# Performance work log

Hardware: AMD Instinct MI355X
Metric: run time of the kernel (lower is better)

Reference implementation:

```python
import jax, jax.numpy as jnp
import numpy as np

N = 50000      # num_nodes
E = 800000     # num_edges
D = 128        # hidden_dim
V = 32000      # vocab_size
T = 8          # num_edge_types
NT = 16        # num_node_types


def setup_inputs() -> dict:
    key = jax.random.key(0)
    ks = jax.random.split(key, 10)
    s = 1.0 / np.sqrt(D)
    return {
        "x": jax.random.randint(ks[0], (N,), 0, V),
        "edge_index": jax.random.randint(ks[1], (2, E), 0, N),
        "edge_type": jax.random.randint(ks[2], (E,), 0, T),
        "node_type": jax.random.randint(ks[3], (N,), 0, NT),
        "emb": jax.random.normal(ks[4], (V, D), dtype=jnp.float32) * s,
        "W_rel": jax.random.normal(ks[5], (T, D, D), dtype=jnp.float32) * s,
        "b_node": jax.random.normal(ks[6], (NT, D), dtype=jnp.float32) * 0.01,
        "W_ih": jax.random.normal(ks[7], (3 * D, D), dtype=jnp.float32) * s,
        "W_hh": jax.random.normal(ks[8], (3 * D, D), dtype=jnp.float32) * s,
        "b_ih": jnp.zeros((3 * D,), dtype=jnp.float32),
        "b_hh": jnp.zeros((3 * D,), dtype=jnp.float32),
    }


def _gru_cell(inp, h, W_ih, W_hh, b_ih, b_hh):
    # torch.nn.GRUCell semantics
    gi = inp @ W_ih.T + b_ih   # [N, 3D]
    gh = h @ W_hh.T + b_hh     # [N, 3D]
    i_r, i_z, i_n = jnp.split(gi, 3, axis=-1)
    h_r, h_z, h_n = jnp.split(gh, 3, axis=-1)
    r = jax.nn.sigmoid(i_r + h_r)
    z = jax.nn.sigmoid(i_z + h_z)
    n = jnp.tanh(i_n + r * h_n)
    return (1.0 - z) * n + z * h


def reference(x, edge_index, edge_type, node_type, emb, W_rel, b_node, W_ih, W_hh, b_ih, b_hh):
    h = emb[x]                                   # [N, D] node embeddings
    src, dst = edge_index[0], edge_index[1]
    n_nodes = h.shape[0]
    for _ in range(5):
        # relational message passing: per-edge-type linear on source nodes
        Ht = jnp.einsum('nd,tdf->ntf', h, W_rel)  # [N, T, D] all-type transforms
        msg = Ht[src, edge_type]                  # [E, D] gather per edge
        aggr = jax.ops.segment_sum(msg, dst, num_segments=n_nodes)  # scatter-add to dst
        aggr = aggr + b_node[node_type]           # node-type-specific bias
        h = _gru_cell(aggr, h, W_ih, W_hh, b_ih, b_hh)
    return h
```

## Files before the change

### kernel.cpp

```cpp
#include <hip/hip_runtime.h>
#include <hip/hip_fp16.h>
#include <math.h>

#define N_NODES 50000
#define N_EDGES 800000
#define D 128
#define T_TYPES 8
#define TPAD 136
#define NBLK_SCAN 196
#define TILES 1563
#define GRID_GRU 512

typedef short short8 __attribute__((ext_vector_type(8)));
typedef unsigned short ushort4v __attribute__((ext_vector_type(4)));
typedef float float4v __attribute__((ext_vector_type(4)));
typedef unsigned short ushort_t;

static __device__ __forceinline__ unsigned short f2bf(float f) {
    unsigned u = __float_as_uint(f);
    u += 0x7fff + ((u >> 16) & 1);
    return (unsigned short)(u >> 16);
}
static __device__ __forceinline__ float bf2f(unsigned short b) {
    return __uint_as_float((unsigned)b << 16);
}
static __device__ __forceinline__ void splitbf(float x, unsigned short& hi, unsigned short& lo) {
    unsigned short h_ = f2bf(x);
    hi = h_;
    lo = f2bf(x - bf2f(h_));
}

#define GLOAD16(gp, lp) __builtin_amdgcn_global_load_lds( \
    (const __attribute__((address_space(1))) unsigned int*)(gp), \
    (__attribute__((address_space(3))) unsigned int*)(lp), 16, 0, 0)

__global__ void embed_gather(const int* __restrict__ x, const float* __restrict__ emb,
                             ushort_t* __restrict__ hhi, ushort_t* __restrict__ hlo) {
    int n = blockIdx.x;
    int d = threadIdx.x;
    float v = emb[(size_t)x[n] * D + d];
    unsigned short a, b;
    splitbf(v, a, b);
    hhi[(size_t)n * D + d] = a;
    hlo[(size_t)n * D + d] = b;
}

__global__ void convert_wrelT(const float* __restrict__ Wrel,
                              ushort_t* __restrict__ hi, ushort_t* __restrict__ lo) {
    int idx = blockIdx.x * 256 + threadIdx.x;
    int t = idx >> 14;
    int rem = idx & 16383;
    int f = rem >> 7;
    int d = rem & 127;
    unsigned short a, b;
    splitbf(Wrel[((size_t)t << 14) + (d << 7) + f], a, b);
    hi[idx] = a;
    lo[idx] = b;
}

__global__ void convert_w(const float* __restrict__ in,
                          ushort_t* __restrict__ hi, ushort_t* __restrict__ lo, int n) {
    int idx = blockIdx.x * 256 + threadIdx.x;
    if (idx < n) {
        unsigned short a, b;
        splitbf(in[idx], a, b);
        hi[idx] = a;
        lo[idx] = b;
    }
}

__global__ void count_deg(const int* __restrict__ ei, int* __restrict__ deg) {
    int e = blockIdx.x * 256 + threadIdx.x;
    if (e >= N_EDGES) return;
    atomicAdd(&deg[ei[N_EDGES + e]], 1);
}

__global__ __launch_bounds__(256) void scan_blocks(const int* __restrict__ deg,
                                                   int* __restrict__ bsums) {
    __shared__ int red[4];
    int idx = blockIdx.x * 256 + threadIdx.x;
    int v = (idx < N_NODES) ? deg[idx] : 0;
#pragma unroll
    for (int o = 32; o > 0; o >>= 1) v += __shfl_down(v, o);
    if ((threadIdx.x & 63) == 0) red[threadIdx.x >> 6] = v;
    __syncthreads();
    if (threadIdx.x == 0) bsums[blockIdx.x] = red[0] + red[1] + red[2] + red[3];
}

__global__ __launch_bounds__(256) void scan_tops(int* __restrict__ bsums) {
    __shared__ int s[256];
    int tid = threadIdx.x;
    int v = (tid < NBLK_SCAN) ? bsums[tid] : 0;
    s[tid] = v;
    __syncthreads();
#pragma unroll
    for (int o = 1; o < 256; o <<= 1) {
        int u = (tid >= o) ? s[tid - o] : 0;
        __syncthreads();
        s[tid] += u;
        __syncthreads();
    }
    if (tid < NBLK_SCAN) bsums[tid] = s[tid] - v;
}

__global__ __launch_bounds__(256) void scan_final(const int* __restrict__ bsums,
                                                  int* __restrict__ deg_cursor,
                                                  int* __restrict__ rs) {
    __shared__ int s[256];
    int tid = threadIdx.x;
    int idx = blockIdx.x * 256 + tid;
    int v = (idx < N_NODES) ? deg_cursor[idx] : 0;
    s[tid] = v;
    __syncthreads();
#pragma unroll
    for (int o = 1; o < 256; o <<= 1) {
        int u = (tid >= o) ? s[tid - o] : 0;
        __syncthreads();
        s[tid] += u;
        __syncthreads();
    }
    int excl = s[tid] - v + bsums[blockIdx.x];
    if (idx < N_NODES) {
        rs[idx] = excl;
        deg_cursor[idx] = excl;
    }
    if (idx == 0) rs[N_NODES] = N_EDGES;
}

__global__ void fill_csr(const int* __restrict__ ei, const int* __restrict__ et,
                         int* __restrict__ cursor, int* __restrict__ packed) {
    int e = blockIdx.x * 256 + threadIdx.x;
    if (e >= N_EDGES) return;
    int dst = ei[N_EDGES + e];
    int pos = atomicAdd(&cursor[dst], 1);
    packed[pos] = (ei[e] << 3) | et[e];
}

__global__ __launch_bounds__(256, 2) void gemm_rel(const ushort_t* __restrict__ hhi,
                                                   const ushort_t* __restrict__ hlo,
                                                   const ushort_t* __restrict__ Whi,
                                                   const ushort_t* __restrict__ Wlo,
                                                   ushort_t* __restrict__ Ht) {
    __shared__ __align__(16) ushort_t wlds[2][128 * TPAD];
    const int tid = threadIdx.x;
    const int wave = tid >> 6, lane = tid & 63;
    const int q = lane >> 4, li = lane & 15;
    const int t = blockIdx.y;
    const int m_base = blockIdx.x * 128 + wave * 32;

    {
        const ushort_t* gh = Whi + ((size_t)t << 14);
        const ushort_t* gl = Wlo + ((size_t)t << 14);
#pragma unroll
        for (int i = 0; i < 8; ++i) {
            int g = (i * 256 + tid) * 8;
            int row = g >> 7, col = g & 127;
            *(short8*)(&wlds[0][row * TPAD + col]) = *(const short8*)(gh + g);
            *(short8*)(&wlds[1][row * TPAD + col]) = *(const short8*)(gl + g);
        }
    }
    __syncthreads();

    int r0 = m_base + li;      if (r0 > N_NODES - 1) r0 = N_NODES - 1;
    int r1 = m_base + 16 + li; if (r1 > N_NODES - 1) r1 = N_NODES - 1;
    const ushort_t* A0h = hhi + (size_t)r0 * D + q * 8;
    const ushort_t* A0l = hlo + (size_t)r0 * D + q * 8;
    const ushort_t* A1h = hhi + (size_t)r1 * D + q * 8;
    const ushort_t* A1l = hlo + (size_t)r1 * D + q * 8;

    short8 a0h[4], a0l[4], a1h[4], a1l[4];
#pragma unroll
    for (int ks = 0; ks < 4; ++ks) {
        a0h[ks] = *(const short8*)(A0h + ks * 32);
        a0l[ks] = *(const short8*)(A0l + ks * 32);
        a1h[ks] = *(const short8*)(A1h + ks * 32);
        a1l[ks] = *(const short8*)(A1l + ks * 32);
    }

    float4v acc[2][8];
#pragma unroll
    for (int m = 0; m < 2; ++m)
#pragma unroll
        for (int ft = 0; ft < 8; ++ft) acc[m][ft] = (float4v){0.f, 0.f, 0.f, 0.f};

#pragma unroll
    for (int ks = 0; ks < 4; ++ks) {
#pragma unroll
        for (int ft = 0; ft < 8; ++ft) {
            const int lo_off = (ft * 16 + li) * TPAD + ks * 32 + q * 8;
            short8 bh = *(const short8*)(&wlds[0][lo_off]);
            short8 bl = *(const short8*)(&wlds[1][lo_off]);
            acc[0][ft] = __builtin_amdgcn_mfma_f32_16x16x32_bf16(a0h[ks], bh, acc[0][ft], 0, 0, 0);
            acc[0][ft] = __builtin_amdgcn_mfma_f32_16x16x32_bf16(a0l[ks], bh, acc[0][ft], 0, 0, 0);
            acc[0][ft] = __builtin_amdgcn_mfma_f32_16x16x32_bf16(a0h[ks], bl, acc[0][ft], 0, 0, 0);
            acc[1][ft] = __builtin_amdgcn_mfma_f32_16x16x32_bf16(a1h[ks], bh, acc[1][ft], 0, 0, 0);
            acc[1][ft] = __builtin_amdgcn_mfma_f32_16x16x32_bf16(a1l[ks], bh, acc[1][ft], 0, 0, 0);
            acc[1][ft] = __builtin_amdgcn_mfma_f32_16x16x32_bf16(a1h[ks], bl, acc[1][ft], 0, 0, 0);
        }
    }

    __syncthreads();
    ushort_t* tw = &wlds[0][0] + wave * 32 * TPAD;
#pragma unroll
    for (int m = 0; m < 2; ++m)
#pragma unroll
        for (int ft = 0; ft < 8; ++ft)
#pragma unroll
            for (int r = 0; r < 4; ++r) {
                __half hv = __float2half_rn(acc[m][ft][r]);
                tw[(m * 16 + q * 4 + r) * TPAD + ft * 16 + li] = __half_as_ushort(hv);
            }
#pragma unroll
    for (int i = 0; i < 8; ++i) {
        int row = i * 4 + q;
        int col = li * 8;
        short8 v = *(const short8*)(tw + row * TPAD + col);
        int orow = m_base + row;
        if (orow < N_NODES)
            *(short8*)(Ht + (size_t)orow * 1024 + (t << 7) + col) = v;
    }
}

__global__ __launch_bounds__(256) void aggregate_csr(const int* __restrict__ rs,
                                                     const int* __restrict__ packed,
                                                     const ushort_t* __restrict__ Ht,
                                                     const int* __restrict__ nt,
                                                     const float* __restrict__ b_node,
                                                     ushort_t* __restrict__ ahi,
                                                     ushort_t* __restrict__ alo) {
    int n = blockIdx.x * 4 + (threadIdx.x >> 6);
    if (n >= N_NODES) return;
    const int lane = threadIdx.x & 63;
    const int beg = rs[n], end = rs[n + 1];
    const __half2* Ht2 = (const __half2*)Ht;

    float2 acc = ((const float2*)(b_node + (size_t)nt[n] * D))[lane];

    int i = beg;
    for (; i + 3 < end; i += 4) {
        int p0 = packed[i], p1 = packed[i + 1], p2 = packed[i + 2], p3 = packed[i + 3];
        float2 f0 = __half22float2(Ht2[(size_t)p0 * 64 + lane]);
        float2 f1 = __half22float2(Ht2[(size_t)p1 * 64 + lane]);
        float2 f2 = __half22float2(Ht2[(size_t)p2 * 64 + lane]);
        float2 f3 = __half22float2(Ht2[(size_t)p3 * 64 + lane]);
        acc.x += (f0.x + f1.x) + (f2.x + f3.x);
        acc.y += (f0.y + f1.y) + (f2.y + f3.y);
    }
    for (; i < end; ++i) {
        int pk = packed[i];
        float2 fv = __half22float2(Ht2[(size_t)pk * 64 + lane]);
        acc.x += fv.x;
        acc.y += fv.y;
    }

    unsigned short h0, l0, h1, l1;
    splitbf(acc.x, h0, l0);
    splitbf(acc.y, h1, l1);
    ((unsigned*)ahi)[(size_t)n * 64 + lane] = (unsigned)h0 | ((unsigned)h1 << 16);
    ((unsigned*)alo)[(size_t)n * 64 + lane] = (unsigned)l0 | ((unsigned)l1 << 16);
}

__global__ __launch_bounds__(512, 2) void gru_persist(
    const ushort_t* __restrict__ ahi, const ushort_t* __restrict__ alo,
    const ushort_t* __restrict__ hhi_in, const ushort_t* __restrict__ hlo_in,
    ushort_t* __restrict__ hhi_out, ushort_t* __restrict__ hlo_out,
    const ushort_t* __restrict__ Wihi, const ushort_t* __restrict__ Wilo,
    const ushort_t* __restrict__ Whhi, const ushort_t* __restrict__ Whlo,
    const float* __restrict__ b_ih, const float* __restrict__ b_hh,
    float* __restrict__ h, int write_h)
{
    __shared__ __align__(16) ushort_t xlds[2][4][4096];

    const int tid = threadIdx.x;
    const int w = tid >> 6, lane = tid & 63;
    const int q = lane >> 4, li = lane & 15;
    const int fg = w * 16 + li;
    const int f0 = w * 16 + q * 4;

    const size_t oR = (size_t)fg * D + q * 8;
    const size_t oZ = (size_t)(D + fg) * D + q * 8;
    const size_t oN = (size_t)(2 * D + fg) * D + q * 8;
    short8 Wr[12][4];
#pragma unroll
    for (int ks = 0; ks < 4; ++ks) {
        const int off = ks * 32;
        Wr[0][ks]  = *(const short8*)(Wihi + oR + off);
        Wr[1][ks]  = *(const short8*)(Wilo + oR + off);
        Wr[2][ks]  = *(const short8*)(Whhi + oR + off);
        Wr[3][ks]  = *(const short8*)(Whlo + oR + off);
        Wr[4][ks]  = *(const short8*)(Wihi + oZ + off);
        Wr[5][ks]  = *(const short8*)(Wilo + oZ + off);
        Wr[6][ks]  = *(const short8*)(Whhi + oZ + off);
        Wr[7][ks]  = *(const short8*)(Whlo + oZ + off);
        Wr[8][ks]  = *(const short8*)(Wihi + oN + off);
        Wr[9][ks]  = *(const short8*)(Wilo + oN + off);
        Wr[10][ks] = *(const short8*)(Whhi + oN + off);
        Wr[11][ks] = *(const short8*)(Whlo + oN + off);
    }
    float4v bR4 = *(const float4v*)(b_ih + f0);
    float4v bZ4 = *(const float4v*)(b_ih + D + f0);
    float4v bIn4 = *(const float4v*)(b_ih + 2 * D + f0);
    {
        float4v t0 = *(const float4v*)(b_hh + f0);
        float4v t1 = *(const float4v*)(b_hh + D + f0);
        bR4 += t0; bZ4 += t1;
    }
    float4v bHn4 = *(const float4v*)(b_hh + 2 * D + f0);

    const int lrow = w * 4 + (lane >> 4);
    const int cswz = (lane & 15) ^ (lrow & 7);

#define STAGE(BUF_, TILE_) do {                                      \
        int gr_ = (TILE_) * 32 + lrow;                               \
        if (gr_ > N_NODES - 1) gr_ = N_NODES - 1;                    \
        const size_t so_ = (size_t)gr_ * D + cswz * 8;               \
        ushort_t* lb_ = &xlds[BUF_][0][0] + (w * 4) * 128;           \
        GLOAD16(ahi + so_,    lb_);                                  \
        GLOAD16(alo + so_,    lb_ + 4096);                           \
        GLOAD16(hhi_in + so_, lb_ + 8192);                           \
        GLOAD16(hlo_in + so_, lb_ + 12288);                          \
    } while (0)

    const int s = blockIdx.x;
    STAGE(0, s);
    __syncthreads();

    int cur = 0;
    for (int tile = s; tile < TILES; tile += GRID_GRU) {
        const int nxt = tile + GRID_GRU;
        if (nxt < TILES) STAGE(cur ^ 1, nxt);

        const ushort_t* xb = &xlds[cur][0][0];
        float4v aR[2], aZ[2], aI[2], aH[2];
#pragma unroll
        for (int m = 0; m < 2; ++m) {
            aR[m] = (float4v){0.f, 0.f, 0.f, 0.f};
            aZ[m] = aR[m]; aI[m] = aR[m]; aH[m] = aR[m];
        }
#pragma unroll
        for (int ks = 0; ks < 4; ++ks) {
#pragma unroll
            for (int m = 0; m < 2; ++m) {
                const int row = m * 16 + li;
                const int inoff = row * 128 + ((ks * 32 + q * 8) ^ ((row & 7) << 3));
                short8 xah = *(const short8*)(xb + inoff);
                short8 xal = *(const short8*)(xb + 4096 + inoff);
                short8 xhh = *(const short8*)(xb + 8192 + inoff);
                short8 xhl = *(const short8*)(xb + 12288 + inoff);
                aR[m] = __builtin_amdgcn_mfma_f32_16x16x32_bf16(Wr[0][ks], xah, aR[m], 0, 0, 0);
                aR[m] = __builtin_amdgcn_mfma_f32_16x16x32_bf16(Wr[0][ks], xal, aR[m], 0, 0, 0);
                aR[m] = __builtin_amdgcn_mfma_f32_16x16x32_bf16(Wr[1][ks], xah, aR[m], 0, 0, 0);
                aR[m] = __builtin_amdgcn_mfma_f32_16x16x32_bf16(Wr[2][ks], xhh, aR[m], 0, 0, 0);
                aR[m] = __builtin_amdgcn_mfma_f32_16x16x32_bf16(Wr[2][ks], xhl, aR[m], 0, 0, 0);
                aR[m] = __builtin_amdgcn_mfma_f32_16x16x32_bf16(Wr[3][ks], xhh, aR[m], 0, 0, 0);
                aZ[m] = __builtin_amdgcn_mfma_f32_16x16x32_bf16(Wr[4][ks], xah, aZ[m], 0, 0, 0);
                aZ[m] = __builtin_amdgcn_mfma_f32_16x16x32_bf16(Wr[4][ks], xal, aZ[m], 0, 0, 0);
                aZ[m] = __builtin_amdgcn_mfma_f32_16x16x32_bf16(Wr[5][ks], xah, aZ[m], 0, 0, 0);
                aZ[m] = __builtin_amdgcn_mfma_f32_16x16x32_bf16(Wr[6][ks], xhh, aZ[m], 0, 0, 0);
                aZ[m] = __builtin_amdgcn_mfma_f32_16x16x32_bf16(Wr[6][ks], xhl, aZ[m], 0, 0, 0);
                aZ[m] = __builtin_amdgcn_mfma_f32_16x16x32_bf16(Wr[7][ks], xhh, aZ[m], 0, 0, 0);
                aI[m] = __builtin_amdgcn_mfma_f32_16x16x32_bf16(Wr[8][ks], xah, aI[m], 0, 0, 0);
                aI[m] = __builtin_amdgcn_mfma_f32_16x16x32_bf16(Wr[8][ks], xal, aI[m], 0, 0, 0);
                aI[m] = __builtin_amdgcn_mfma_f32_16x16x32_bf16(Wr[9][ks], xah, aI[m], 0, 0, 0);
                aH[m] = __builtin_amdgcn_mfma_f32_16x16x32_bf16(Wr[10][ks], xhh, aH[m], 0, 0, 0);
                aH[m] = __builtin_amdgcn_mfma_f32_16x16x32_bf16(Wr[10][ks], xhl, aH[m], 0, 0, 0);
                aH[m] = __builtin_amdgcn_mfma_f32_16x16x32_bf16(Wr[11][ks], xhh, aH[m], 0, 0, 0);
            }
        }

#pragma unroll
        for (int m = 0; m < 2; ++m) {
            const int node = tile * 32 + m * 16 + li;
            const int row = m * 16 + li;
            const int chunk = (f0 >> 3) ^ (row & 7);
            const int hoff = row * 128 + chunk * 8 + (q & 1) * 4;
            ushort4v hh4 = *(const ushort4v*)(xb + 8192 + hoff);
            ushort4v hl4 = *(const ushort4v*)(xb + 12288 + hoff);
            if (node < N_NODES) {
                ushort4v sh4, sl4;
                float4v hn4;
#pragma unroll
                for (int r = 0; r < 4; ++r) {
                    float hold = bf2f(hh4[r]) + bf2f(hl4[r]);
                    float rg = 1.0f / (1.0f + __expf(-(aR[m][r] + bR4[r])));
                    float zg = 1.0f / (1.0f + __expf(-(aZ[m][r] + bZ4[r])));
                    float narg = aI[m][r] + bIn4[r] + rg * (aH[m][r] + bHn4[r]);
                    float ex = __expf(2.0f * narg);
                    float ng = 1.0f - 2.0f / (ex + 1.0f);
                    float hn = (1.0f - zg) * ng + zg * hold;
                    hn4[r] = hn;
                    unsigned short sh, sl;
                    splitbf(hn, sh, sl);
                    sh4[r] = sh;
                    sl4[r] = sl;
                }
                const size_t go = (size_t)node * D + f0;
                *(ushort4v*)(hhi_out + go) = sh4;
                *(ushort4v*)(hlo_out + go) = sl4;
                if (write_h) *(float4v*)(h + go) = hn4;
            }
        }
        __syncthreads();
        cur ^= 1;
    }
#undef STAGE
}

extern "C" void kernel_launch(void* const* d_in, const int* in_sizes, int n_in,
                              void* d_out, int out_size, void* d_ws, size_t ws_size,
                              hipStream_t stream) {
    const int* x      = (const int*)d_in[0];
    const int* ei     = (const int*)d_in[1];
    const int* et     = (const int*)d_in[2];
    const int* nt     = (const int*)d_in[3];
    const float* emb  = (const float*)d_in[4];
    const float* Wrel = (const float*)d_in[5];
    const float* b_node = (const float*)d_in[6];
    const float* W_ih = (const float*)d_in[7];
    const float* W_hh = (const float*)d_in[8];
    const float* b_ih = (const float*)d_in[9];
    const float* b_hh = (const float*)d_in[10];

    float* h = (float*)d_out;
    float* ws = (float*)d_ws;

    ushort_t* Ht = (ushort_t*)ws;
    ushort_t* us = (ushort_t*)(ws + 25600000);
    ushort_t* ahi  = us;
    ushort_t* alo  = us + 6400000;
    ushort_t* hhi  = us + 12800000;
    ushort_t* hlo  = us + 19200000;
    ushort_t* Whi  = us + 25600000;
    ushort_t* Wlo  = Whi + 131072;
    ushort_t* Wihi = Wlo + 131072;
    ushort_t* Wilo = Wihi + 49152;
    ushort_t* Whhi = Wilo + 49152;
    ushort_t* Whlo = Whhi + 49152;
    int* rs     = (int*)(ws + 38629376);
    int* packed = rs + 50004;
    int* bsums  = packed + 800000;
    ushort_t* hhi2 = (ushort_t*)(ws + 39479808);
    ushort_t* hlo2 = hhi2 + 6400000;
    int* deg    = (int*)ws;

    convert_wrelT<<<512, 256, 0, stream>>>(Wrel, Whi, Wlo);
    convert_w<<<192, 256, 0, stream>>>(W_ih, Wihi, Wilo, 3 * D * D);
    convert_w<<<192, 256, 0, stream>>>(W_hh, Whhi, Whlo, 3 * D * D);
    embed_gather<<<N_NODES, 128, 0, stream>>>(x, emb, hhi, hlo);

    hipMemsetAsync(deg, 0, 50000 * sizeof(int), stream);
    count_deg<<<3125, 256, 0, stream>>>(ei, deg);
    scan_blocks<<<NBLK_SCAN, 256, 0, stream>>>(deg, bsums);
    scan_tops<<<1, 256, 0, stream>>>(bsums);
    scan_final<<<NBLK_SCAN, 256, 0, stream>>>(bsums, deg, rs);
    fill_csr<<<3125, 256, 0, stream>>>(ei, et, deg, packed);

    for (int it = 0; it < 5; ++it) {
        const ushort_t* hi_in = (it & 1) ? hhi2 : hhi;
        const ushort_t* lo_in = (it & 1) ? hlo2 : hlo;
        ushort_t* hi_out = (it & 1) ? hhi : hhi2;
        ushort_t* lo_out = (it & 1) ? hlo : hlo2;
        dim3 g(391, T_TYPES);
        gemm_rel<<<g, 256, 0, stream>>>(hi_in, lo_in, Whi, Wlo, Ht);
        aggregate_csr<<<12500, 256, 0, stream>>>(rs, packed, Ht, nt, b_node, ahi, alo);
        gru_persist<<<GRID_GRU, 512, 0, stream>>>(ahi, alo, hi_in, lo_in, hi_out, lo_out,
                                                  Wihi, Wilo, Whhi, Whlo, b_ih, b_hh,
                                                  h, it == 4 ? 1 : 0);
    }
}
```

Before: 1.055 ms.

## Store Ht in type-major planes, drop LDS staging in relational GEMM and GRU

The per-type transform output Ht moves from node-major [N,T,D] to type-major planes [T,N,D], and the CSR packed edge index becomes et*N+src so the aggregation gather addresses the new layout directly. The relational GEMM no longer stages W_rel into LDS; it reads weight fragments straight from global/cache, which shrinks LDS so the launch bound can allow 4 blocks per CU. The persistent double-buffered GRU kernel with register-resident weights is replaced by a non-persistent 2D grid that reloads weights and inputs from global memory per tile. The aim is higher occupancy and less LDS/sync overhead, at the cost of more global/L2 traffic for weights.

```diff
diff --git a/kernel.cpp b/kernel.cpp
--- a/kernel.cpp
+++ b/kernel.cpp
@@ -9,7 +9,7 @@
 #define TPAD 136
 #define NBLK_SCAN 196
 #define TILES 1563
-#define GRID_GRU 512
+#define HT_PLANE 6400000
 
 typedef short short8 __attribute__((ext_vector_type(8)));
 typedef unsigned short ushort4v __attribute__((ext_vector_type(4)));
@@ -29,10 +29,6 @@
     hi = h_;
     lo = f2bf(x - bf2f(h_));
 }
-
-#define GLOAD16(gp, lp) __builtin_amdgcn_global_load_lds( \
-    (const __attribute__((address_space(1))) unsigned int*)(gp), \
-    (__attribute__((address_space(3))) unsigned int*)(lp), 16, 0, 0)
 
 __global__ void embed_gather(const int* __restrict__ x, const float* __restrict__ emb,
                              ushort_t* __restrict__ hhi, ushort_t* __restrict__ hlo) {
@@ -133,33 +129,20 @@
     if (e >= N_EDGES) return;
     int dst = ei[N_EDGES + e];
     int pos = atomicAdd(&cursor[dst], 1);
-    packed[pos] = (ei[e] << 3) | et[e];
-}
-
-__global__ __launch_bounds__(256, 2) void gemm_rel(const ushort_t* __restrict__ hhi,
+    packed[pos] = et[e] * N_NODES + ei[e];
+}
+
+__global__ __launch_bounds__(256, 4) void gemm_rel(const ushort_t* __restrict__ hhi,
                                                    const ushort_t* __restrict__ hlo,
                                                    const ushort_t* __restrict__ Whi,
                                                    const ushort_t* __restrict__ Wlo,
                                                    ushort_t* __restrict__ Ht) {
-    __shared__ __align__(16) ushort_t wlds[2][128 * TPAD];
+    __shared__ __align__(16) ushort_t twb[4][32 * TPAD];
     const int tid = threadIdx.x;
     const int wave = tid >> 6, lane = tid & 63;
     const int q = lane >> 4, li = lane & 15;
     const int t = blockIdx.y;
     const int m_base = blockIdx.x * 128 + wave * 32;
-
-    {
-        const ushort_t* gh = Whi + ((size_t)t << 14);
-        const ushort_t* gl = Wlo + ((size_t)t << 14);
-#pragma unroll
-        for (int i = 0; i < 8; ++i) {
-            int g = (i * 256 + tid) * 8;
-            int row = g >> 7, col = g & 127;
-            *(short8*)(&wlds[0][row * TPAD + col]) = *(const short8*)(gh + g);
-            *(short8*)(&wlds[1][row * TPAD + col]) = *(const short8*)(gl + g);
-        }
-    }
-    __syncthreads();
 
     int r0 = m_base + li;      if (r0 > N_NODES - 1) r0 = N_NODES - 1;
     int r1 = m_base + 16 + li; if (r1 > N_NODES - 1) r1 = N_NODES - 1;
@@ -183,13 +166,15 @@
 #pragma unroll
         for (int ft = 0; ft < 8; ++ft) acc[m][ft] = (float4v){0.f, 0.f, 0.f, 0.f};
 
+    const ushort_t* Wth = Whi + ((size_t)t << 14);
+    const ushort_t* Wtl = Wlo + ((size_t)t << 14);
 #pragma unroll
     for (int ks = 0; ks < 4; ++ks) {
 #pragma unroll
         for (int ft = 0; ft < 8; ++ft) {
-            const int lo_off = (ft * 16 + li) * TPAD + ks * 32 + q * 8;
-            short8 bh = *(const short8*)(&wlds[0][lo_off]);
-            short8 bl = *(const short8*)(&wlds[1][lo_off]);
+            const int wo = (ft * 16 + li) * 128 + ks * 32 + q * 8;
+            short8 bh = *(const short8*)(Wth + wo);
+            short8 bl = *(const short8*)(Wtl + wo);
             acc[0][ft] = __builtin_amdgcn_mfma_f32_16x16x32_bf16(a0h[ks], bh, acc[0][ft], 0, 0, 0);
             acc[0][ft] = __builtin_amdgcn_mfma_f32_16x16x32_bf16(a0l[ks], bh, acc[0][ft], 0, 0, 0);
             acc[0][ft] = __builtin_amdgcn_mfma_f32_16x16x32_bf16(a0h[ks], bl, acc[0][ft], 0, 0, 0);
@@ -199,8 +184,7 @@
         }
     }
 
-    __syncthreads();
-    ushort_t* tw = &wlds[0][0] + wave * 32 * TPAD;
+    ushort_t* tw = &twb[wave][0];
 #pragma unroll
     for (int m = 0; m < 2; ++m)
 #pragma unroll
@@ -217,7 +201,7 @@
         short8 v = *(const short8*)(tw + row * TPAD + col);
         int orow = m_base + row;
         if (orow < N_NODES)
-            *(short8*)(Ht + (size_t)orow * 1024 + (t << 7) + col) = v;
+            *(short8*)(Ht + (size_t)t * HT_PLANE + (size_t)orow * D + col) = v;
     }
 }
 
@@ -260,7 +244,7 @@
     ((unsigned*)alo)[(size_t)n * 64 + lane] = (unsigned)l0 | ((unsigned)l1 << 16);
 }
 
-__global__ __launch_bounds__(512, 2) void gru_persist(
+__global__ __launch_bounds__(256, 4) void gru_direct(
     const ushort_t* __restrict__ ahi, const ushort_t* __restrict__ alo,
     const ushort_t* __restrict__ hhi_in, const ushort_t* __restrict__ hlo_in,
     ushort_t* __restrict__ hhi_out, ushort_t* __restrict__ hlo_out,
@@ -269,34 +253,17 @@
     const float* __restrict__ b_ih, const float* __restrict__ b_hh,
     float* __restrict__ h, int write_h)
 {
-    __shared__ __align__(16) ushort_t xlds[2][4][4096];
-
     const int tid = threadIdx.x;
     const int w = tid >> 6, lane = tid & 63;
     const int q = lane >> 4, li = lane & 15;
-    const int fg = w * 16 + li;
-    const int f0 = w * 16 + q * 4;
+    const int fg = blockIdx.y * 64 + w * 16 + li;
+    const int f0 = blockIdx.y * 64 + w * 16 + q * 4;
+    const int n0 = blockIdx.x * 32;
 
     const size_t oR = (size_t)fg * D + q * 8;
     const size_t oZ = (size_t)(D + fg) * D + q * 8;
     const size_t oN = (size_t)(2 * D + fg) * D + q * 8;
-    short8 Wr[12][4];
-#pragma unroll
-    for (int ks = 0; ks < 4; ++ks) {
-        const int off = ks * 32;
-        Wr[0][ks]  = *(const short8*)(Wihi + oR + off);
-        Wr[1][ks]  = *(const short8*)(Wilo + oR + off);
-        Wr[2][ks]  = *(const short8*)(Whhi + oR + off);
-        Wr[3][ks]  = *(const short8*)(Whlo + oR + off);
-        Wr[4][ks]  = *(const short8*)(Wihi + oZ + off);
-        Wr[5][ks]  = *(const short8*)(Wilo + oZ + off);
-        Wr[6][ks]  = *(const short8*)(Whhi + oZ + off);
-        Wr[7][ks]  = *(const short8*)(Whlo + oZ + off);
-        Wr[8][ks]  = *(const short8*)(Wihi + oN + off);
-        Wr[9][ks]  = *(const short8*)(Wilo + oN + off);
-        Wr[10][ks] = *(const short8*)(Whhi + oN + off);
-        Wr[11][ks] = *(const short8*)(Whlo + oN + off);
-    }
+
     float4v bR4 = *(const float4v*)(b_ih + f0);
     float4v bZ4 = *(const float4v*)(b_ih + D + f0);
     float4v bIn4 = *(const float4v*)(b_ih + 2 * D + f0);
@@ -307,103 +274,110 @@
     }
     float4v bHn4 = *(const float4v*)(b_hh + 2 * D + f0);
 
-    const int lrow = w * 4 + (lane >> 4);
-    const int cswz = (lane & 15) ^ (lrow & 7);
-
-#define STAGE(BUF_, TILE_) do {                                      \
-        int gr_ = (TILE_) * 32 + lrow;                               \
-        if (gr_ > N_NODES - 1) gr_ = N_NODES - 1;                    \
-        const size_t so_ = (size_t)gr_ * D + cswz * 8;               \
-        ushort_t* lb_ = &xlds[BUF_][0][0] + (w * 4) * 128;           \
-        GLOAD16(ahi + so_,    lb_);                                  \
-        GLOAD16(alo + so_,    lb_ + 4096);                           \
-        GLOAD16(hhi_in + so_, lb_ + 8192);                           \
-        GLOAD16(hlo_in + so_, lb_ + 12288);                          \
-    } while (0)
-
-    const int s = blockIdx.x;
-    STAGE(0, s);
-    __syncthreads();
-
-    int cur = 0;
-    for (int tile = s; tile < TILES; tile += GRID_GRU) {
-        const int nxt = tile + GRID_GRU;
-        if (nxt < TILES) STAGE(cur ^ 1, nxt);
-
-        const ushort_t* xb = &xlds[cur][0][0];
-        float4v aR[2], aZ[2], aI[2], aH[2];
-#pragma unroll
-        for (int m = 0; m < 2; ++m) {
-            aR[m] = (float4v){0.f, 0.f, 0.f, 0.f};
-            aZ[m] = aR[m]; aI[m] = aR[m]; aH[m] = aR[m];
+    int r0 = n0 + li;      if (r0 > N_NODES - 1) r0 = N_NODES - 1;
+    int r1 = n0 + 16 + li; if (r1 > N_NODES - 1) r1 = N_NODES - 1;
+    const size_t xo0 = (size_t)r0 * D + q * 8;
+    const size_t xo1 = (size_t)r1 * D + q * 8;
+
+    float4v aR[2], aZ[2], aI[2], aH[2];
+#pragma unroll
+    for (int m = 0; m < 2; ++m) {
+        aR[m] = (float4v){0.f, 0.f, 0.f, 0.f};
+        aZ[m] = aR[m]; aI[m] = aR[m]; aH[m] = aR[m];
+    }
+
+#pragma unroll
+    for (int ks = 0; ks < 4; ++ks) {
+        const int off = ks * 32;
+        short8 x0ah = *(const short8*)(ahi + xo0 + off);
+        short8 x0al = *(const short8*)(alo + xo0 + off);
+        short8 x0hh = *(const short8*)(hhi_in + xo0 + off);
+        short8 x0hl = *(const short8*)(hlo_in + xo0 + off);
+        short8 x1ah = *(const short8*)(ahi + xo1 + off);
+        short8 x1al = *(const short8*)(alo + xo1 + off);
+        short8 x1hh = *(const short8*)(hhi_in + xo1 + off);
+        short8 x1hl = *(const short8*)(hlo_in + xo1 + off);
+        short8 wIRh = *(const short8*)(Wihi + oR + off);
+        short8 wIRl = *(const short8*)(Wilo + oR + off);
+        short8 wHRh = *(const short8*)(Whhi + oR + off);
+        short8 wHRl = *(const short8*)(Whlo + oR + off);
+        short8 wIZh = *(const short8*)(Wihi + oZ + off);
+        short8 wIZl = *(const short8*)(Wilo + oZ + off);
+        short8 wHZh = *(const short8*)(Whhi + oZ + off);
+        short8 wHZl = *(const short8*)(Whlo + oZ + off);
+        short8 wINh = *(const short8*)(Wihi + oN + off);
+        short8 wINl = *(const short8*)(Wilo + oN + off);
+        short8 wHNh = *(const short8*)(Whhi + oN + off);
+        short8 wHNl = *(const short8*)(Whlo + oN + off);
+
+        aR[0] = __builtin_amdgcn_mfma_f32_16x16x32_bf16(wIRh, x0ah, aR[0], 0, 0, 0);
+        aR[0] = __builtin_amdgcn_mfma_f32_16x16x32_bf16(wIRh, x0al, aR[0], 0, 0, 0);
+        aR[0] = __builtin_amdgcn_mfma_f32_16x16x32_bf16(wIRl, x0ah, aR[0], 0, 0, 0);
+        aR[0] = __builtin_amdgcn_mfma_f32_16x16x32_bf16(wHRh, x0hh, aR[0], 0, 0, 0);
+        aR[0] = __builtin_amdgcn_mfma_f32_16x16x32_bf16(wHRh, x0hl, aR[0], 0, 0, 0);
+        aR[0] = __builtin_amdgcn_mfma_f32_16x16x32_bf16(wHRl, x0hh, aR[0], 0, 0, 0);
+        aZ[0] = __builtin_amdgcn_mfma_f32_16x16x32_bf16(wIZh, x0ah, aZ[0], 0, 0, 0);
+        aZ[0] = __builtin_amdgcn_mfma_f32_16x16x32_bf16(wIZh, x0al, aZ[0], 0, 0, 0);
+        aZ[0] = __builtin_amdgcn_mfma_f32_16x16x32_bf16(wIZl, x0ah, aZ[0], 0, 0, 0);
+        aZ[0] = __builtin_amdgcn_mfma_f32_16x16x32_bf16(wHZh, x0hh, aZ[0], 0, 0, 0);
+        aZ[0] = __builtin_amdgcn_mfma_f32_16x16x32_bf16(wHZh, x0hl, aZ[0], 0, 0, 0);
+        aZ[0] = __builtin_amdgcn_mfma_f32_16x16x32_bf16(wHZl, x0hh, aZ[0], 0, 0, 0);
+        aI[0] = __builtin_amdgcn_mfma_f32_16x16x32_bf16(wINh, x0ah, aI[0], 0, 0, 0);
+        aI[0] = __builtin_amdgcn_mfma_f32_16x16x32_bf16(wINh, x0al, aI[0], 0, 0, 0);
+        aI[0] = __builtin_amdgcn_mfma_f32_16x16x32_bf16(wINl, x0ah, aI[0], 0, 0, 0);
+        aH[0] = __builtin_amdgcn_mfma_f32_16x16x32_bf16(wHNh, x0hh, aH[0], 0, 0, 0);
+        aH[0] = __builtin_amdgcn_mfma_f32_16x16x32_bf16(wHNh, x0hl, aH[0], 0, 0, 0);
+        aH[0] = __builtin_amdgcn_mfma_f32_16x16x32_bf16(wHNl, x0hh, aH[0], 0, 0, 0);
+
+        aR[1] = __builtin_amdgcn_mfma_f32_16x16x32_bf16(wIRh, x1ah, aR[1], 0, 0, 0);
+        aR[1] = __builtin_amdgcn_mfma_f32_16x16x32_bf16(wIRh, x1al, aR[1], 0, 0, 0);
+        aR[1] = __builtin_amdgcn_mfma_f32_16x16x32_bf16(wIRl, x1ah, aR[1], 0, 0, 0);
+        aR[1] = __builtin_amdgcn_mfma_f32_16x16x32_bf16(wHRh, x1hh, aR[1], 0, 0, 0);
+        aR[1] = __builtin_amdgcn_mfma_f32_16x16x32_bf16(wHRh, x1hl, aR[1], 0, 0, 0);
+        aR[1] = __builtin_amdgcn_mfma_f32_16x16x32_bf16(wHRl, x1hh, aR[1], 0, 0, 0);
+        aZ[1] = __builtin_amdgcn_mfma_f32_16x16x32_bf16(wIZh, x1ah, aZ[1], 0, 0, 0);
+        aZ[1] = __builtin_amdgcn_mfma_f32_16x16x32_bf16(wIZh, x1al, aZ[1], 0, 0, 0);
+        aZ[1] = __builtin_amdgcn_mfma_f32_16x16x32_bf16(wIZl, x1ah, aZ[1], 0, 0, 0);
+        aZ[1] = __builtin_amdgcn_mfma_f32_16x16x32_bf16(wHZh, x1hh, aZ[1], 0, 0, 0);
+        aZ[1] = __builtin_amdgcn_mfma_f32_16x16x32_bf16(wHZh, x1hl, aZ[1], 0, 0, 0);
+        aZ[1] = __builtin_amdgcn_mfma_f32_16x16x32_bf16(wHZl, x1hh, aZ[1], 0, 0, 0);
+        aI[1] = __builtin_amdgcn_mfma_f32_16x16x32_bf16(wINh, x1ah, aI[1], 0, 0, 0);
+        aI[1] = __builtin_amdgcn_mfma_f32_16x16x32_bf16(wINh, x1al, aI[1], 0, 0, 0);
+        aI[1] = __builtin_amdgcn_mfma_f32_16x16x32_bf16(wINl, x1ah, aI[1], 0, 0, 0);
+        aH[1] = __builtin_amdgcn_mfma_f32_16x16x32_bf16(wHNh, x1hh, aH[1], 0, 0, 0);
+        aH[1] = __builtin_amdgcn_mfma_f32_16x16x32_bf16(wHNh, x1hl, aH[1], 0, 0, 0);
+        aH[1] = __builtin_amdgcn_mfma_f32_16x16x32_bf16(wHNl, x1hh, aH[1], 0, 0, 0);
+    }
+
+#pragma unroll
+    for (int m = 0; m < 2; ++m) {
+        const int node = n0 + m * 16 + li;
+        if (node < N_NODES) {
+            const size_t go = (size_t)node * D + f0;
+            ushort4v hh4 = *(const ushort4v*)(hhi_in + go);
+            ushort4v hl4 = *(const ushort4v*)(hlo_in + go);
+            ushort4v sh4, sl4;
+            float4v hn4;
+#pragma unroll
+            for (int r = 0; r < 4; ++r) {
+                float hold = bf2f(hh4[r]) + bf2f(hl4[r]);
+                float rg = 1.0f / (1.0f + __expf(-(aR[m][r] + bR4[r])));
+                float zg = 1.0f / (1.0f + __expf(-(aZ[m][r] + bZ4[r])));
+                float narg = aI[m][r] + bIn4[r] + rg * (aH[m][r] + bHn4[r]);
+                float ex = __expf(2.0f * narg);
+                float ng = 1.0f - 2.0f / (ex + 1.0f);
+                float hn = (1.0f - zg) * ng + zg * hold;
+                hn4[r] = hn;
+                unsigned short sh, sl;
+                splitbf(hn, sh, sl);
+                sh4[r] = sh;
+                sl4[r] = sl;
+            }
+            *(ushort4v*)(hhi_out + go) = sh4;
+            *(ushort4v*)(hlo_out + go) = sl4;
+            if (write_h) *(float4v*)(h + go) = hn4;
         }
-#pragma unroll
-        for (int ks = 0; ks < 4; ++ks) {
-#pragma unroll
-            for (int m = 0; m < 2; ++m) {
-                const int row = m * 16 + li;
-                const int inoff = row * 128 + ((ks * 32 + q * 8) ^ ((row & 7) << 3));
-                short8 xah = *(const short8*)(xb + inoff);
-                short8 xal = *(const short8*)(xb + 4096 + inoff);
-                short8 xhh = *(const short8*)(xb + 8192 + inoff);
-                short8 xhl = *(const short8*)(xb + 12288 + inoff);
-                aR[m] = __builtin_amdgcn_mfma_f32_16x16x32_bf16(Wr[0][ks], xah, aR[m], 0, 0, 0);
-                aR[m] = __builtin_amdgcn_mfma_f32_16x16x32_bf16(Wr[0][ks], xal, aR[m], 0, 0, 0);
-                aR[m] = __builtin_amdgcn_mfma_f32_16x16x32_bf16(Wr[1][ks], xah, aR[m], 0, 0, 0);
-                aR[m] = __builtin_amdgcn_mfma_f32_16x16x32_bf16(Wr[2][ks], xhh, aR[m], 0, 0, 0);
-                aR[m] = __builtin_amdgcn_mfma_f32_16x16x32_bf16(Wr[2][ks], xhl, aR[m], 0, 0, 0);
-                aR[m] = __builtin_amdgcn_mfma_f32_16x16x32_bf16(Wr[3][ks], xhh, aR[m], 0, 0, 0);
-                aZ[m] = __builtin_amdgcn_mfma_f32_16x16x32_bf16(Wr[4][ks], xah, aZ[m], 0, 0, 0);
-                aZ[m] = __builtin_amdgcn_mfma_f32_16x16x32_bf16(Wr[4][ks], xal, aZ[m], 0, 0, 0);
-                aZ[m] = __builtin_amdgcn_mfma_f32_16x16x32_bf16(Wr[5][ks], xah, aZ[m], 0, 0, 0);
-                aZ[m] = __builtin_amdgcn_mfma_f32_16x16x32_bf16(Wr[6][ks], xhh, aZ[m], 0, 0, 0);
-                aZ[m] = __builtin_amdgcn_mfma_f32_16x16x32_bf16(Wr[6][ks], xhl, aZ[m], 0, 0, 0);
-                aZ[m] = __builtin_amdgcn_mfma_f32_16x16x32_bf16(Wr[7][ks], xhh, aZ[m], 0, 0, 0);
-                aI[m] = __builtin_amdgcn_mfma_f32_16x16x32_bf16(Wr[8][ks], xah, aI[m], 0, 0, 0);
-                aI[m] = __builtin_amdgcn_mfma_f32_16x16x32_bf16(Wr[8][ks], xal, aI[m], 0, 0, 0);
-                aI[m] = __builtin_amdgcn_mfma_f32_16x16x32_bf16(Wr[9][ks], xah, aI[m], 0, 0, 0);
-                aH[m] = __builtin_amdgcn_mfma_f32_16x16x32_bf16(Wr[10][ks], xhh, aH[m], 0, 0, 0);
-                aH[m] = __builtin_amdgcn_mfma_f32_16x16x32_bf16(Wr[10][ks], xhl, aH[m], 0, 0, 0);
-                aH[m] = __builtin_amdgcn_mfma_f32_16x16x32_bf16(Wr[11][ks], xhh, aH[m], 0, 0, 0);
-            }
-        }
-
-#pragma unroll
-        for (int m = 0; m < 2; ++m) {
-            const int node = tile * 32 + m * 16 + li;
-            const int row = m * 16 + li;
-            const int chunk = (f0 >> 3) ^ (row & 7);
-            const int hoff = row * 128 + chunk * 8 + (q & 1) * 4;
-            ushort4v hh4 = *(const ushort4v*)(xb + 8192 + hoff);
-            ushort4v hl4 = *(const ushort4v*)(xb + 12288 + hoff);
-            if (node < N_NODES) {
-                ushort4v sh4, sl4;
-                float4v hn4;
-#pragma unroll
-                for (int r = 0; r < 4; ++r) {
-                    float hold = bf2f(hh4[r]) + bf2f(hl4[r]);
-                    float rg = 1.0f / (1.0f + __expf(-(aR[m][r] + bR4[r])));
-                    float zg = 1.0f / (1.0f + __expf(-(aZ[m][r] + bZ4[r])));
-                    float narg = aI[m][r] + bIn4[r] + rg * (aH[m][r] + bHn4[r]);
-                    float ex = __expf(2.0f * narg);
-                    float ng = 1.0f - 2.0f / (ex + 1.0f);
-                    float hn = (1.0f - zg) * ng + zg * hold;
-                    hn4[r] = hn;
-                    unsigned short sh, sl;
-                    splitbf(hn, sh, sl);
-                    sh4[r] = sh;
-                    sl4[r] = sl;
-                }
-                const size_t go = (size_t)node * D + f0;
-                *(ushort4v*)(hhi_out + go) = sh4;
-                *(ushort4v*)(hlo_out + go) = sl4;
-                if (write_h) *(float4v*)(h + go) = hn4;
-            }
-        }
-        __syncthreads();
-        cur ^= 1;
-    }
-#undef STAGE
+    }
 }
 
 extern "C" void kernel_launch(void* const* d_in, const int* in_sizes, int n_in,
@@ -463,8 +437,9 @@
         dim3 g(391, T_TYPES);
         gemm_rel<<<g, 256, 0, stream>>>(hi_in, lo_in, Whi, Wlo, Ht);
         aggregate_csr<<<12500, 256, 0, stream>>>(rs, packed, Ht, nt, b_node, ahi, alo);
-        gru_persist<<<GRID_GRU, 512, 0, stream>>>(ahi, alo, hi_in, lo_in, hi_out, lo_out,
-                                                  Wihi, Wilo, Whhi, Whlo, b_ih, b_hh,
-                                                  h, it == 4 ? 1 : 0);
-    }
-}
+        dim3 gg(TILES, 2);
+        gru_direct<<<gg, 256, 0, stream>>>(ahi, alo, hi_in, lo_in, hi_out, lo_out,
+                                           Wihi, Wilo, Whhi, Whlo, b_ih, b_hh,
+                                           h, it == 4 ? 1 : 0);
+    }
+}
```

New measurement: 1.708 ms. 1.62x slower.
